# Optimization experiments

Measured on AMD Instinct MI355X. Metric: run time of the kernel, lower is better.

## Reference

```python
import jax, jax.numpy as jnp
import numpy as np

N_HEAD = 16
LN_EPS = 1e-5


def setup_inputs() -> dict:
    key = jax.random.key(0)
    ks = jax.random.split(key, 12)
    B, S, D = 4, 1024, 1024
    s = 1.0 / np.sqrt(D)
    return {
        "Q": jax.random.normal(ks[0], (B, S, D), jnp.float32),
        "K": jax.random.normal(ks[1], (B, S, D), jnp.float32),
        "V": jax.random.normal(ks[2], (B, S, D), jnp.float32),
        # Linear weights stored torch-style [out, in]
        "Wq": jax.random.normal(ks[3], (D, D), jnp.float32) * s,
        "bq": jnp.zeros((D,), jnp.float32),
        "Wk": jax.random.normal(ks[4], (D, D), jnp.float32) * s,
        "bk": jnp.zeros((D,), jnp.float32),
        "Wv": jax.random.normal(ks[5], (D, D), jnp.float32) * s,
        "bv": jnp.zeros((D,), jnp.float32),
        "Wo": jax.random.normal(ks[6], (D, D), jnp.float32) * s,
        "bo": jnp.zeros((D,), jnp.float32),
        "ln_g": jnp.ones((D,), jnp.float32),
        "ln_b": jnp.zeros((D,), jnp.float32),
    }


def _layer_norm(x, g, b):
    mu = jnp.mean(x, axis=-1, keepdims=True)
    var = jnp.mean(jnp.square(x - mu), axis=-1, keepdims=True)
    return (x - mu) * jax.lax.rsqrt(var + LN_EPS) * g + b


def reference(Q, K, V, Wq, bq, Wk, bk, Wv, bv, Wo, bo, ln_g, ln_b):
    B, S, D = Q.shape
    H = N_HEAD
    dk = D // H
    # projections, split heads: [B, H, S, dk]
    q = (Q @ Wq.T + bq).reshape(B, S, H, dk).transpose(0, 2, 1, 3)
    k = (K @ Wk.T + bk).reshape(B, S, H, dk).transpose(0, 2, 1, 3)
    v = (V @ Wv.T + bv).reshape(B, S, H, dk).transpose(0, 2, 1, 3)
    scores = jnp.einsum("bhqd,bhkd->bhqk", q, k) / np.sqrt(dk)
    # NOTE: original module applies softmax twice (F.softmax then nn.Softmax)
    attn = jax.nn.softmax(jax.nn.softmax(scores, axis=-1), axis=-1)
    ctx = jnp.einsum("bhqk,bhkd->bhqd", attn, v)  # [B, H, S, dk]
    ctx = ctx.transpose(0, 2, 1, 3).reshape(B, S, D)
    out = ctx @ Wo.T + bo
    return _layer_norm(out + Q, ln_g, ln_b)
```

## Files before the change

kernel.cpp:

```cpp
#include <hip/hip_runtime.h>
#include <cstdint>
#include <cstddef>


typedef unsigned short ushort_t;
typedef __attribute__((ext_vector_type(8))) short bf16x8;
typedef __attribute__((ext_vector_type(8))) unsigned short us8;
typedef __attribute__((ext_vector_type(4))) unsigned short us4;
typedef __attribute__((ext_vector_type(4))) float f32x4;

#define MFMA16(a, b, c) __builtin_amdgcn_mfma_f32_16x16x32_bf16((a), (b), (c), 0, 0, 0)

__device__ __forceinline__ float b2f(ushort_t u) {
  union { unsigned int i; float f; } x; x.i = ((unsigned int)u) << 16; return x.f;
}
__device__ __forceinline__ ushort_t f2b(float f) {
  union { unsigned int i; float f; } x; x.f = f;
  unsigned int r = (x.i + 0x7FFFu + ((x.i >> 16) & 1u)) >> 16;
  return (ushort_t)r;
}
__device__ __forceinline__ us8 cvt8(float4 a, float4 b) {
  us8 r;
  r[0] = f2b(a.x); r[1] = f2b(a.y); r[2] = f2b(a.z); r[3] = f2b(a.w);
  r[4] = f2b(b.x); r[5] = f2b(b.y); r[6] = f2b(b.z); r[7] = f2b(b.w);
  return r;
}

__device__ __forceinline__ void gll16(const ushort_t* g, ushort_t* l) {
  __builtin_amdgcn_global_load_lds(
      (const __attribute__((address_space(1))) void*)g,
      (__attribute__((address_space(3))) void*)l, 16, 0, 0);
}

__global__ __launch_bounds__(256, 8) void cvt4_kernel(
    const float* __restrict__ w0, const float* __restrict__ w1,
    const float* __restrict__ w2, const float* __restrict__ w3,
    ushort_t* __restrict__ dst) {
  const int which = blockIdx.y;
  const float* src = (which == 0) ? w0 : (which == 1) ? w1 : (which == 2) ? w2 : w3;
  const int i = (blockIdx.x * 256 + threadIdx.x) * 8;
  const float4 a = *(const float4*)(src + i);
  const float4 b = *(const float4*)(src + i + 4);
  *(us8*)(dst + (size_t)which * 1048576 + i) = cvt8(a, b);
}

__global__ __launch_bounds__(256, 3) void qkv_proj_kernel(
    const float* __restrict__ Qin, const float* __restrict__ Kin,
    const float* __restrict__ Vin,
    const ushort_t* __restrict__ wq, const ushort_t* __restrict__ wk,
    const ushort_t* __restrict__ wv,
    const float* __restrict__ bq, const float* __restrict__ bk,
    const float* __restrict__ bv,
    ushort_t* __restrict__ qb, ushort_t* __restrict__ kb,
    ushort_t* __restrict__ vb) {
  __shared__ __align__(16) ushort_t Asl[128 * 32];
  __shared__ __align__(16) ushort_t Bsl[128 * 32];
  const float* A; const ushort_t* W; const float* bias; float scale;
  if (blockIdx.z == 0)      { A = Qin; W = wq; bias = bq; scale = 0.125f; }
  else if (blockIdx.z == 1) { A = Kin; W = wk; bias = bk; scale = 1.0f; }
  else                      { A = Vin; W = wv; bias = bv; scale = 1.0f; }
  const int l = blockIdx.x;
  const int xcd = l & 7, ii = l >> 3;
  const int m0 = (xcd * 4 + (ii >> 3)) * 128;
  const int n0 = (ii & 7) * 128;
  const int tid = threadIdx.x;
  const int wave = tid >> 6, lane = tid & 63;
  const int l15 = lane & 15, quad = lane >> 4;
  const int wr = wave >> 1, wc = wave & 1;

  const int ra = tid >> 2, ca = (tid & 3) * 8;
  const float* Ap0 = A + (size_t)(m0 + ra) * 1024 + ca;
  const float* Ap1 = A + (size_t)(m0 + ra + 64) * 1024 + ca;

  const int rB0 = wave * 32 + (lane >> 2);
  const ushort_t* Bg0 = W + (size_t)(n0 + rB0) * 1024 + (lane & 3) * 8;
  const ushort_t* Bg1 = W + (size_t)(n0 + rB0 + 16) * 1024 + (lane & 3) * 8;
  ushort_t* Bl0 = Bsl + wave * 1024;
  ushort_t* Bl1 = Bsl + wave * 1024 + 512;

  float4 a00 = *(const float4*)(Ap0), a01 = *(const float4*)(Ap0 + 4);
  float4 a10 = *(const float4*)(Ap1), a11 = *(const float4*)(Ap1 + 4);

  f32x4 acc[4][4] = {};
  for (int k0 = 0; k0 < 1024; k0 += 32) {
    __syncthreads();
    *(us8*)(Asl + ra * 32 + ca) = cvt8(a00, a01);
    *(us8*)(Asl + (ra + 64) * 32 + ca) = cvt8(a10, a11);
    gll16(Bg0 + k0, Bl0);
    gll16(Bg1 + k0, Bl1);
    __syncthreads();
    if (k0 + 32 < 1024) {
      a00 = *(const float4*)(Ap0 + k0 + 32); a01 = *(const float4*)(Ap0 + k0 + 36);
      a10 = *(const float4*)(Ap1 + k0 + 32); a11 = *(const float4*)(Ap1 + k0 + 36);
    }
    bf16x8 af[4], bfr[4];
#pragma unroll
    for (int s = 0; s < 4; ++s)
      af[s] = *(const bf16x8*)(Asl + (wr * 64 + s * 16 + l15) * 32 + quad * 8);
#pragma unroll
    for (int s = 0; s < 4; ++s)
      bfr[s] = *(const bf16x8*)(Bsl + (wc * 64 + s * 16 + l15) * 32 + quad * 8);
#pragma unroll
    for (int ms = 0; ms < 4; ++ms)
#pragma unroll
      for (int ns = 0; ns < 4; ++ns)
        acc[ms][ns] = MFMA16(af[ms], bfr[ns], acc[ms][ns]);
  }

  if (blockIdx.z != 2) {
    ushort_t* outp = (blockIdx.z == 0) ? qb : kb;
#pragma unroll
    for (int ns = 0; ns < 4; ++ns) {
      const int col = n0 + wc * 64 + ns * 16 + l15;
      const float bv_ = bias[col];
#pragma unroll
      for (int ms = 0; ms < 4; ++ms) {
        const int rowb = m0 + wr * 64 + ms * 16 + quad * 4;
#pragma unroll
        for (int r = 0; r < 4; ++r) {
          outp[(size_t)(rowb + r) * 1024 + col] =
              f2b((acc[ms][ns][r] + bv_) * scale);
        }
      }
    }
  } else {
#pragma unroll
    for (int ns = 0; ns < 4; ++ns) {
      const int col = n0 + wc * 64 + ns * 16 + l15;
      const float bv_ = bias[col];
      const int h = col >> 6, d = col & 63;
#pragma unroll
      for (int ms = 0; ms < 4; ++ms) {
        const int i0 = m0 + wr * 64 + ms * 16 + quad * 4;
        const int b = i0 >> 10, s0 = i0 & 1023;
        us4 pack;
#pragma unroll
        for (int r = 0; r < 4; ++r) pack[r] = f2b(acc[ms][ns][r] + bv_);
        *(us4*)(vb + ((size_t)(b * 16 + h) * 64 + d) * 1024 + s0) = pack;
      }
    }
  }
}

__global__ __launch_bounds__(256, 4) void attn_kernel(
    const ushort_t* __restrict__ qb, const ushort_t* __restrict__ kb,
    const ushort_t* __restrict__ vb, ushort_t* __restrict__ ctx) {
  __shared__ __align__(16) ushort_t Qs[64 * 72];
  __shared__ __align__(16) ushort_t Ks[64 * 72];
  __shared__ __align__(16) ushort_t Vt[64 * 72];
  __shared__ __align__(16) ushort_t Ps[4][16 * 68];

  const int tid = threadIdx.x, wave = tid >> 6, lane = tid & 63;
  const int l15 = lane & 15, quad = lane >> 4;
  const int l = blockIdx.x;
  const int xcd = l & 7, ii = l >> 3;
  const int bh = xcd * 8 + (ii >> 4);
  const int q0 = (ii & 15) * 64;
  const int b = bh >> 4, h = bh & 15;
  const ushort_t* qg = qb + ((size_t)b << 20) + h * 64;
  const ushort_t* kg = kb + ((size_t)b << 20) + h * 64;
  const ushort_t* vg = vb + ((size_t)bh << 16);

  const int kr0 = tid >> 3, kc0 = (tid & 7) * 8;
  const int kr1 = (tid + 256) >> 3, kc1 = kc0;

  *(us8*)(Qs + kr0 * 72 + kc0) = *(const us8*)(qg + (size_t)(q0 + kr0) * 1024 + kc0);
  *(us8*)(Qs + kr1 * 72 + kc1) = *(const us8*)(qg + (size_t)(q0 + kr1) * 1024 + kc1);

  float z1[4] = {0.f, 0.f, 0.f, 0.f};
  us8 rk0 = *(const us8*)(kg + (size_t)kr0 * 1024 + kc0);
  us8 rk1 = *(const us8*)(kg + (size_t)kr1 * 1024 + kc1);
  for (int kt = 0; kt < 16; ++kt) {
    __syncthreads();
    *(us8*)(Ks + kr0 * 72 + kc0) = rk0;
    *(us8*)(Ks + kr1 * 72 + kc1) = rk1;
    __syncthreads();
    if (kt < 15) {
      rk0 = *(const us8*)(kg + (size_t)((kt + 1) * 64 + kr0) * 1024 + kc0);
      rk1 = *(const us8*)(kg + (size_t)((kt + 1) * 64 + kr1) * 1024 + kc1);
    }
    f32x4 sc[4] = {};
#pragma unroll
    for (int kk = 0; kk < 2; ++kk) {
      const bf16x8 aq = *(const bf16x8*)(Qs + (wave * 16 + l15) * 72 + kk * 32 + quad * 8);
#pragma unroll
      for (int ns = 0; ns < 4; ++ns) {
        const bf16x8 bk_ = *(const bf16x8*)(Ks + (ns * 16 + l15) * 72 + kk * 32 + quad * 8);
        sc[ns] = MFMA16(aq, bk_, sc[ns]);
      }
    }
#pragma unroll
    for (int ns = 0; ns < 4; ++ns)
#pragma unroll
      for (int r = 0; r < 4; ++r) z1[r] += __expf(sc[ns][r]);
  }
  float iz1[4];
#pragma unroll
  for (int r = 0; r < 4; ++r) {
    float s = z1[r];
#pragma unroll
    for (int off = 1; off < 16; off <<= 1) s += __shfl_xor(s, off, 64);
    iz1[r] = 1.0f / s;
  }

  f32x4 oac[4] = {};
  float z2[4] = {0.f, 0.f, 0.f, 0.f};
  rk0 = *(const us8*)(kg + (size_t)kr0 * 1024 + kc0);
  rk1 = *(const us8*)(kg + (size_t)kr1 * 1024 + kc1);
  us8 rv0 = *(const us8*)(vg + (size_t)kr0 * 1024 + kc0);
  us8 rv1 = *(const us8*)(vg + (size_t)kr1 * 1024 + kc1);
  for (int kt = 0; kt < 16; ++kt) {
    __syncthreads();
    *(us8*)(Ks + kr0 * 72 + kc0) = rk0;
    *(us8*)(Ks + kr1 * 72 + kc1) = rk1;
    *(us8*)(Vt + kr0 * 72 + kc0) = rv0;
    *(us8*)(Vt + kr1 * 72 + kc1) = rv1;
    __syncthreads();
    if (kt < 15) {
      rk0 = *(const us8*)(kg + (size_t)((kt + 1) * 64 + kr0) * 1024 + kc0);
      rk1 = *(const us8*)(kg + (size_t)((kt + 1) * 64 + kr1) * 1024 + kc1);
      rv0 = *(const us8*)(vg + (size_t)kr0 * 1024 + (kt + 1) * 64 + kc0);
      rv1 = *(const us8*)(vg + (size_t)kr1 * 1024 + (kt + 1) * 64 + kc1);
    }
    f32x4 sc[4] = {};
#pragma unroll
    for (int kk = 0; kk < 2; ++kk) {
      const bf16x8 aq = *(const bf16x8*)(Qs + (wave * 16 + l15) * 72 + kk * 32 + quad * 8);
#pragma unroll
      for (int ns = 0; ns < 4; ++ns) {
        const bf16x8 bk_ = *(const bf16x8*)(Ks + (ns * 16 + l15) * 72 + kk * 32 + quad * 8);
        sc[ns] = MFMA16(aq, bk_, sc[ns]);
      }
    }
#pragma unroll
    for (int ns = 0; ns < 4; ++ns)
#pragma unroll
      for (int r = 0; r < 4; ++r) {
        const float p1 = __expf(sc[ns][r]) * iz1[r];
        const float e2 = __expf(p1);
        z2[r] += e2;
        Ps[wave][(quad * 4 + r) * 68 + ns * 16 + l15] = f2b(e2);
      }
    __asm__ __volatile__("s_waitcnt lgkmcnt(0)" ::: "memory");
#pragma unroll
    for (int kk = 0; kk < 2; ++kk) {
      const ushort_t* pp = &Ps[wave][l15 * 68 + kk * 32 + quad * 8];
      union { us4 hseg[2]; bf16x8 v; } u;
      u.hseg[0] = *(const us4*)pp;
      u.hseg[1] = *(const us4*)(pp + 4);
      const bf16x8 ap = u.v;
#pragma unroll
      for (int ns2 = 0; ns2 < 4; ++ns2) {
        const bf16x8 bv_ = *(const bf16x8*)(Vt + (ns2 * 16 + l15) * 72 + kk * 32 + quad * 8);
        oac[ns2] = MFMA16(ap, bv_, oac[ns2]);
      }
    }
  }

#pragma unroll
  for (int r = 0; r < 4; ++r) {
    float s = z2[r];
#pragma unroll
    for (int off = 1; off < 16; off <<= 1) s += __shfl_xor(s, off, 64);
    z2[r] = s;
  }
#pragma unroll
  for (int ns2 = 0; ns2 < 4; ++ns2) {
    const int d = ns2 * 16 + l15;
#pragma unroll
    for (int r = 0; r < 4; ++r) {
      const int s = q0 + wave * 16 + quad * 4 + r;
      ctx[((size_t)(b * 1024 + s)) * 1024 + h * 64 + d] = f2b(oac[ns2][r] / z2[r]);
    }
  }
}

__global__ __launch_bounds__(256, 3) void out_proj_kernel(
    const ushort_t* __restrict__ ctxp, const ushort_t* __restrict__ wo,
    const float* __restrict__ bo, ushort_t* __restrict__ pre) {
  __shared__ __align__(16) ushort_t Asl[128 * 32];
  __shared__ __align__(16) ushort_t Bsl[128 * 32];
  const int tid = threadIdx.x;
  const int wave = tid >> 6, lane = tid & 63;
  const int l15 = lane & 15, quad = lane >> 4;
  const int wr = wave >> 1, wc = wave & 1;
  const int l = blockIdx.x;
  const int xcd = l & 7, ii = l >> 3;
  const int m0 = (xcd * 4 + (ii >> 3)) * 128;
  const int n0 = (ii & 7) * 128;

  const int rr = wave * 32 + (lane >> 2);
  const int cc = (lane & 3) * 8;
  const ushort_t* Ag0 = ctxp + (size_t)(m0 + rr) * 1024 + cc;
  const ushort_t* Ag1 = ctxp + (size_t)(m0 + rr + 16) * 1024 + cc;
  const ushort_t* Bg0 = wo + (size_t)(n0 + rr) * 1024 + cc;
  const ushort_t* Bg1 = wo + (size_t)(n0 + rr + 16) * 1024 + cc;
  ushort_t* Al0 = Asl + wave * 1024;
  ushort_t* Al1 = Asl + wave * 1024 + 512;
  ushort_t* Bl0 = Bsl + wave * 1024;
  ushort_t* Bl1 = Bsl + wave * 1024 + 512;

  f32x4 acc[4][4] = {};
  for (int k0 = 0; k0 < 1024; k0 += 32) {
    __syncthreads();
    gll16(Ag0 + k0, Al0);
    gll16(Ag1 + k0, Al1);
    gll16(Bg0 + k0, Bl0);
    gll16(Bg1 + k0, Bl1);
    __syncthreads();
    bf16x8 af[4], bfr[4];
#pragma unroll
    for (int s = 0; s < 4; ++s)
      af[s] = *(const bf16x8*)(Asl + (wr * 64 + s * 16 + l15) * 32 + quad * 8);
#pragma unroll
    for (int s = 0; s < 4; ++s)
      bfr[s] = *(const bf16x8*)(Bsl + (wc * 64 + s * 16 + l15) * 32 + quad * 8);
#pragma unroll
    for (int ms = 0; ms < 4; ++ms)
#pragma unroll
      for (int ns = 0; ns < 4; ++ns)
        acc[ms][ns] = MFMA16(af[ms], bfr[ns], acc[ms][ns]);
  }

#pragma unroll
  for (int ns = 0; ns < 4; ++ns) {
    const int col = n0 + wc * 64 + ns * 16 + l15;
    const float bv_ = bo[col];
#pragma unroll
    for (int ms = 0; ms < 4; ++ms) {
      const int rowb = m0 + wr * 64 + ms * 16 + quad * 4;
#pragma unroll
      for (int r = 0; r < 4; ++r) {
        pre[(size_t)(rowb + r) * 1024 + col] = f2b(acc[ms][ns][r] + bv_);
      }
    }
  }
}

__global__ __launch_bounds__(256, 4) void ln_kernel(
    const ushort_t* __restrict__ pre, const float* __restrict__ Q,
    const float* __restrict__ g, const float* __restrict__ bta,
    float* __restrict__ out) {
  const int row = blockIdx.x;
  const int tid = threadIdx.x;
  const size_t base = (size_t)row * 1024 + tid * 4;
  const ushort4 p4 = *(const ushort4*)(pre + base);
  const float4 q4 = *(const float4*)(Q + base);
  float v[4] = {b2f(p4.x) + q4.x, b2f(p4.y) + q4.y,
                b2f(p4.z) + q4.z, b2f(p4.w) + q4.w};
  float s1 = v[0] + v[1] + v[2] + v[3];
  float s2 = v[0]*v[0] + v[1]*v[1] + v[2]*v[2] + v[3]*v[3];
#pragma unroll
  for (int off = 1; off < 64; off <<= 1) {
    s1 += __shfl_xor(s1, off, 64);
    s2 += __shfl_xor(s2, off, 64);
  }
  __shared__ float r1[4], r2[4];
  const int wave = tid >> 6, lane = tid & 63;
  if (lane == 0) { r1[wave] = s1; r2[wave] = s2; }
  __syncthreads();
  const float t1 = r1[0] + r1[1] + r1[2] + r1[3];
  const float t2 = r2[0] + r2[1] + r2[2] + r2[3];
  const float mu = t1 * (1.0f / 1024.0f);
  const float var = t2 * (1.0f / 1024.0f) - mu * mu;
  const float inv = rsqrtf(var + 1e-5f);
  const int c0 = tid * 4;
#pragma unroll
  for (int j = 0; j < 4; ++j) {
    const int c = c0 + j;
    out[(size_t)row * 1024 + c] = (v[j] - mu) * inv * g[c] + bta[c];
  }
}

extern "C" void kernel_launch(void* const* d_in, const int* in_sizes, int n_in,
                              void* d_out, int out_size, void* d_ws, size_t ws_size,
                              hipStream_t stream) {
  const float* Q  = (const float*)d_in[0];
  const float* K  = (const float*)d_in[1];
  const float* V  = (const float*)d_in[2];
  const float* Wq = (const float*)d_in[3];
  const float* bq = (const float*)d_in[4];
  const float* Wk = (const float*)d_in[5];
  const float* bk = (const float*)d_in[6];
  const float* Wv = (const float*)d_in[7];
  const float* bv = (const float*)d_in[8];
  const float* Wo = (const float*)d_in[9];
  const float* bo = (const float*)d_in[10];
  const float* lg = (const float*)d_in[11];
  const float* lb = (const float*)d_in[12];

  char* ws = (char*)d_ws;
  ushort_t* qb  = (ushort_t*)(ws);
  ushort_t* kb  = (ushort_t*)(ws + ((size_t)8  << 20));
  ushort_t* vb  = (ushort_t*)(ws + ((size_t)16 << 20));
  ushort_t* pre = (ushort_t*)(ws);

  ushort_t* dptr  = (ushort_t*)d_out;
  ushort_t* wo_bf = dptr;
  ushort_t* wq_bf = dptr + 1048576;
  ushort_t* wk_bf = dptr + 2097152;
  ushort_t* wv_bf = dptr + 3145728;
  ushort_t* ctx   = dptr + 4194304;
  float*    out   = (float*)d_out;

  cvt4_kernel<<<dim3(512, 4), 256, 0, stream>>>(Wo, Wq, Wk, Wv, dptr);
  qkv_proj_kernel<<<dim3(256, 1, 3), 256, 0, stream>>>(Q, K, V, wq_bf, wk_bf, wv_bf,
                                                       bq, bk, bv, qb, kb, vb);
  attn_kernel<<<dim3(1024), 256, 0, stream>>>(qb, kb, vb, ctx);
  out_proj_kernel<<<dim3(256), 256, 0, stream>>>(ctx, wo_bf, bo, pre);
  ln_kernel<<<dim3(4096), 256, 0, stream>>>(pre, Q, lg, lb, out);
}
```

Before: 247.0 us.

## Double-buffer projection GEMMs, use exp2 softmax, hoist Q fragments, shrink out-proj tiles

The QKV and output projection GEMMs now use two LDS buffers with 64-wide k steps, so the next tile loads while the current one is computed and one barrier per stage is dropped. The output projection tile shrinks to 64x128 with twice as many blocks and a higher occupancy hint, which spreads work over more CUs. The attention kernel folds log2(e) into the Q scale and first-softmax normaliser so it can call hardware exp2 directly, and it keeps the Q MFMA fragments in registers instead of re-reading them from LDS every iteration. Double buffering doubles LDS per block and adds register pressure, which may lower occupancy.

```diff
diff --git a/kernel.cpp b/kernel.cpp
--- a/kernel.cpp
+++ b/kernel.cpp
@@ -10,6 +10,8 @@
 typedef __attribute__((ext_vector_type(4))) float f32x4;
 
 #define MFMA16(a, b, c) __builtin_amdgcn_mfma_f32_16x16x32_bf16((a), (b), (c), 0, 0, 0)
+#define EXP2F(x) __builtin_amdgcn_exp2f(x)
+#define LOG2E 1.4426950408889634f
 
 __device__ __forceinline__ float b2f(ushort_t u) {
   union { unsigned int i; float f; } x; x.i = ((unsigned int)u) << 16; return x.f;
@@ -53,10 +55,12 @@
     const float* __restrict__ bv,
     ushort_t* __restrict__ qb, ushort_t* __restrict__ kb,
     ushort_t* __restrict__ vb) {
-  __shared__ __align__(16) ushort_t Asl[128 * 32];
-  __shared__ __align__(16) ushort_t Bsl[128 * 32];
+  __shared__ __align__(16) ushort_t Asl0[128 * 32];
+  __shared__ __align__(16) ushort_t Asl1[128 * 32];
+  __shared__ __align__(16) ushort_t Bsl0[128 * 32];
+  __shared__ __align__(16) ushort_t Bsl1[128 * 32];
   const float* A; const ushort_t* W; const float* bias; float scale;
-  if (blockIdx.z == 0)      { A = Qin; W = wq; bias = bq; scale = 0.125f; }
+  if (blockIdx.z == 0)      { A = Qin; W = wq; bias = bq; scale = 0.125f * LOG2E; }
   else if (blockIdx.z == 1) { A = Kin; W = wk; bias = bk; scale = 1.0f; }
   else                      { A = Vin; W = wv; bias = bv; scale = 1.0f; }
   const int l = blockIdx.x;
@@ -72,40 +76,59 @@
   const float* Ap0 = A + (size_t)(m0 + ra) * 1024 + ca;
   const float* Ap1 = A + (size_t)(m0 + ra + 64) * 1024 + ca;
 
-  const int rB0 = wave * 32 + (lane >> 2);
-  const ushort_t* Bg0 = W + (size_t)(n0 + rB0) * 1024 + (lane & 3) * 8;
-  const ushort_t* Bg1 = W + (size_t)(n0 + rB0 + 16) * 1024 + (lane & 3) * 8;
-  ushort_t* Bl0 = Bsl + wave * 1024;
-  ushort_t* Bl1 = Bsl + wave * 1024 + 512;
-
-  float4 a00 = *(const float4*)(Ap0), a01 = *(const float4*)(Ap0 + 4);
-  float4 a10 = *(const float4*)(Ap1), a11 = *(const float4*)(Ap1 + 4);
+  const ushort_t* Bg0 = W + (size_t)(n0 + wave * 32 + (lane >> 2)) * 1024 + (lane & 3) * 8;
+  const ushort_t* Bg1 = W + (size_t)(n0 + wave * 32 + 16 + (lane >> 2)) * 1024 + (lane & 3) * 8;
+
+  float4 xa0 = *(const float4*)(Ap0), xa1 = *(const float4*)(Ap0 + 4);
+  float4 xa2 = *(const float4*)(Ap1), xa3 = *(const float4*)(Ap1 + 4);
+  gll16(Bg0, Bsl0 + wave * 1024);
+  gll16(Bg1, Bsl0 + wave * 1024 + 512);
+  *(us8*)(Asl0 + ra * 32 + ca) = cvt8(xa0, xa1);
+  *(us8*)(Asl0 + (ra + 64) * 32 + ca) = cvt8(xa2, xa3);
+  float4 ya0 = *(const float4*)(Ap0 + 32), ya1 = *(const float4*)(Ap0 + 36);
+  float4 ya2 = *(const float4*)(Ap1 + 32), ya3 = *(const float4*)(Ap1 + 36);
+  __syncthreads();
 
   f32x4 acc[4][4] = {};
-  for (int k0 = 0; k0 < 1024; k0 += 32) {
-    __syncthreads();
-    *(us8*)(Asl + ra * 32 + ca) = cvt8(a00, a01);
-    *(us8*)(Asl + (ra + 64) * 32 + ca) = cvt8(a10, a11);
-    gll16(Bg0 + k0, Bl0);
-    gll16(Bg1 + k0, Bl1);
-    __syncthreads();
-    if (k0 + 32 < 1024) {
-      a00 = *(const float4*)(Ap0 + k0 + 32); a01 = *(const float4*)(Ap0 + k0 + 36);
-      a10 = *(const float4*)(Ap1 + k0 + 32); a11 = *(const float4*)(Ap1 + k0 + 36);
-    }
-    bf16x8 af[4], bfr[4];
-#pragma unroll
-    for (int s = 0; s < 4; ++s)
-      af[s] = *(const bf16x8*)(Asl + (wr * 64 + s * 16 + l15) * 32 + quad * 8);
-#pragma unroll
-    for (int s = 0; s < 4; ++s)
-      bfr[s] = *(const bf16x8*)(Bsl + (wc * 64 + s * 16 + l15) * 32 + quad * 8);
-#pragma unroll
-    for (int ms = 0; ms < 4; ++ms)
-#pragma unroll
-      for (int ns = 0; ns < 4; ++ns)
-        acc[ms][ns] = MFMA16(af[ms], bfr[ns], acc[ms][ns]);
-  }
+#define QKV_COMPUTE(ASL, BSL)                                                   \
+  {                                                                             \
+    bf16x8 af[4], bfr[4];                                                       \
+    _Pragma("unroll") for (int s = 0; s < 4; ++s)                               \
+        af[s] = *(const bf16x8*)((ASL) + (wr * 64 + s * 16 + l15) * 32 + quad * 8); \
+    _Pragma("unroll") for (int s = 0; s < 4; ++s)                               \
+        bfr[s] = *(const bf16x8*)((BSL) + (wc * 64 + s * 16 + l15) * 32 + quad * 8); \
+    _Pragma("unroll") for (int ms = 0; ms < 4; ++ms)                            \
+        _Pragma("unroll") for (int ns = 0; ns < 4; ++ns)                        \
+            acc[ms][ns] = MFMA16(af[ms], bfr[ns], acc[ms][ns]);                 \
+  }
+
+  for (int k0 = 0; k0 < 1024; k0 += 64) {
+    {
+      gll16(Bg0 + k0 + 32, Bsl1 + wave * 1024);
+      gll16(Bg1 + k0 + 32, Bsl1 + wave * 1024 + 512);
+      *(us8*)(Asl1 + ra * 32 + ca) = cvt8(ya0, ya1);
+      *(us8*)(Asl1 + (ra + 64) * 32 + ca) = cvt8(ya2, ya3);
+    }
+    if (k0 + 64 < 1024) {
+      xa0 = *(const float4*)(Ap0 + k0 + 64); xa1 = *(const float4*)(Ap0 + k0 + 68);
+      xa2 = *(const float4*)(Ap1 + k0 + 64); xa3 = *(const float4*)(Ap1 + k0 + 68);
+    }
+    QKV_COMPUTE(Asl0, Bsl0)
+    __syncthreads();
+    if (k0 + 64 < 1024) {
+      gll16(Bg0 + k0 + 64, Bsl0 + wave * 1024);
+      gll16(Bg1 + k0 + 64, Bsl0 + wave * 1024 + 512);
+      *(us8*)(Asl0 + ra * 32 + ca) = cvt8(xa0, xa1);
+      *(us8*)(Asl0 + (ra + 64) * 32 + ca) = cvt8(xa2, xa3);
+      if (k0 + 96 < 1024) {
+        ya0 = *(const float4*)(Ap0 + k0 + 96); ya1 = *(const float4*)(Ap0 + k0 + 100);
+        ya2 = *(const float4*)(Ap1 + k0 + 96); ya3 = *(const float4*)(Ap1 + k0 + 100);
+      }
+    }
+    QKV_COMPUTE(Asl1, Bsl1)
+    __syncthreads();
+  }
+#undef QKV_COMPUTE
 
   if (blockIdx.z != 2) {
     ushort_t* outp = (blockIdx.z == 0) ? qb : kb;
@@ -166,6 +189,10 @@
 
   *(us8*)(Qs + kr0 * 72 + kc0) = *(const us8*)(qg + (size_t)(q0 + kr0) * 1024 + kc0);
   *(us8*)(Qs + kr1 * 72 + kc1) = *(const us8*)(qg + (size_t)(q0 + kr1) * 1024 + kc1);
+  __syncthreads();
+  bf16x8 aqh[2];
+  aqh[0] = *(const bf16x8*)(Qs + (wave * 16 + l15) * 72 + quad * 8);
+  aqh[1] = *(const bf16x8*)(Qs + (wave * 16 + l15) * 72 + 32 + quad * 8);
 
   float z1[4] = {0.f, 0.f, 0.f, 0.f};
   us8 rk0 = *(const us8*)(kg + (size_t)kr0 * 1024 + kc0);
@@ -182,17 +209,16 @@
     f32x4 sc[4] = {};
 #pragma unroll
     for (int kk = 0; kk < 2; ++kk) {
-      const bf16x8 aq = *(const bf16x8*)(Qs + (wave * 16 + l15) * 72 + kk * 32 + quad * 8);
 #pragma unroll
       for (int ns = 0; ns < 4; ++ns) {
         const bf16x8 bk_ = *(const bf16x8*)(Ks + (ns * 16 + l15) * 72 + kk * 32 + quad * 8);
-        sc[ns] = MFMA16(aq, bk_, sc[ns]);
+        sc[ns] = MFMA16(aqh[kk], bk_, sc[ns]);
       }
     }
 #pragma unroll
     for (int ns = 0; ns < 4; ++ns)
 #pragma unroll
-      for (int r = 0; r < 4; ++r) z1[r] += __expf(sc[ns][r]);
+      for (int r = 0; r < 4; ++r) z1[r] += EXP2F(sc[ns][r]);
   }
   float iz1[4];
 #pragma unroll
@@ -200,7 +226,7 @@
     float s = z1[r];
 #pragma unroll
     for (int off = 1; off < 16; off <<= 1) s += __shfl_xor(s, off, 64);
-    iz1[r] = 1.0f / s;
+    iz1[r] = LOG2E / s;
   }
 
   f32x4 oac[4] = {};
@@ -225,19 +251,18 @@
     f32x4 sc[4] = {};
 #pragma unroll
     for (int kk = 0; kk < 2; ++kk) {
-      const bf16x8 aq = *(const bf16x8*)(Qs + (wave * 16 + l15) * 72 + kk * 32 + quad * 8);
 #pragma unroll
       for (int ns = 0; ns < 4; ++ns) {
         const bf16x8 bk_ = *(const bf16x8*)(Ks + (ns * 16 + l15) * 72 + kk * 32 + quad * 8);
-        sc[ns] = MFMA16(aq, bk_, sc[ns]);
+        sc[ns] = MFMA16(aqh[kk], bk_, sc[ns]);
       }
     }
 #pragma unroll
     for (int ns = 0; ns < 4; ++ns)
 #pragma unroll
       for (int r = 0; r < 4; ++r) {
-        const float p1 = __expf(sc[ns][r]) * iz1[r];
-        const float e2 = __expf(p1);
+        const float p1 = EXP2F(sc[ns][r]) * iz1[r];
+        const float e2 = EXP2F(p1);
         z2[r] += e2;
         Ps[wave][(quad * 4 + r) * 68 + ns * 16 + l15] = f2b(e2);
       }
@@ -275,60 +300,69 @@
   }
 }
 
-__global__ __launch_bounds__(256, 3) void out_proj_kernel(
+__global__ __launch_bounds__(256, 4) void out_proj_kernel(
     const ushort_t* __restrict__ ctxp, const ushort_t* __restrict__ wo,
     const float* __restrict__ bo, ushort_t* __restrict__ pre) {
-  __shared__ __align__(16) ushort_t Asl[128 * 32];
-  __shared__ __align__(16) ushort_t Bsl[128 * 32];
+  __shared__ __align__(16) ushort_t Asl0[64 * 32];
+  __shared__ __align__(16) ushort_t Asl1[64 * 32];
+  __shared__ __align__(16) ushort_t Bsl0[128 * 32];
+  __shared__ __align__(16) ushort_t Bsl1[128 * 32];
   const int tid = threadIdx.x;
   const int wave = tid >> 6, lane = tid & 63;
   const int l15 = lane & 15, quad = lane >> 4;
   const int wr = wave >> 1, wc = wave & 1;
   const int l = blockIdx.x;
   const int xcd = l & 7, ii = l >> 3;
-  const int m0 = (xcd * 4 + (ii >> 3)) * 128;
+  const int m0 = (xcd * 8 + (ii >> 3)) * 64;
   const int n0 = (ii & 7) * 128;
 
-  const int rr = wave * 32 + (lane >> 2);
-  const int cc = (lane & 3) * 8;
-  const ushort_t* Ag0 = ctxp + (size_t)(m0 + rr) * 1024 + cc;
-  const ushort_t* Ag1 = ctxp + (size_t)(m0 + rr + 16) * 1024 + cc;
-  const ushort_t* Bg0 = wo + (size_t)(n0 + rr) * 1024 + cc;
-  const ushort_t* Bg1 = wo + (size_t)(n0 + rr + 16) * 1024 + cc;
-  ushort_t* Al0 = Asl + wave * 1024;
-  ushort_t* Al1 = Asl + wave * 1024 + 512;
-  ushort_t* Bl0 = Bsl + wave * 1024;
-  ushort_t* Bl1 = Bsl + wave * 1024 + 512;
-
-  f32x4 acc[4][4] = {};
-  for (int k0 = 0; k0 < 1024; k0 += 32) {
-    __syncthreads();
-    gll16(Ag0 + k0, Al0);
-    gll16(Ag1 + k0, Al1);
-    gll16(Bg0 + k0, Bl0);
-    gll16(Bg1 + k0, Bl1);
-    __syncthreads();
-    bf16x8 af[4], bfr[4];
-#pragma unroll
-    for (int s = 0; s < 4; ++s)
-      af[s] = *(const bf16x8*)(Asl + (wr * 64 + s * 16 + l15) * 32 + quad * 8);
-#pragma unroll
-    for (int s = 0; s < 4; ++s)
-      bfr[s] = *(const bf16x8*)(Bsl + (wc * 64 + s * 16 + l15) * 32 + quad * 8);
-#pragma unroll
-    for (int ms = 0; ms < 4; ++ms)
-#pragma unroll
-      for (int ns = 0; ns < 4; ++ns)
-        acc[ms][ns] = MFMA16(af[ms], bfr[ns], acc[ms][ns]);
-  }
+  const ushort_t* Ag = ctxp + (size_t)(m0 + wave * 16 + (lane >> 2)) * 1024 + (lane & 3) * 8;
+  const ushort_t* Bg0 = wo + (size_t)(n0 + wave * 32 + (lane >> 2)) * 1024 + (lane & 3) * 8;
+  const ushort_t* Bg1 = wo + (size_t)(n0 + wave * 32 + 16 + (lane >> 2)) * 1024 + (lane & 3) * 8;
+
+  gll16(Ag, Asl0 + wave * 512);
+  gll16(Bg0, Bsl0 + wave * 1024);
+  gll16(Bg1, Bsl0 + wave * 1024 + 512);
+  __syncthreads();
+
+  f32x4 acc[2][4] = {};
+#define OUTP_COMPUTE(ASL, BSL)                                                  \
+  {                                                                             \
+    bf16x8 af[2], bfr[4];                                                       \
+    _Pragma("unroll") for (int s = 0; s < 2; ++s)                               \
+        af[s] = *(const bf16x8*)((ASL) + (wr * 32 + s * 16 + l15) * 32 + quad * 8); \
+    _Pragma("unroll") for (int s = 0; s < 4; ++s)                               \
+        bfr[s] = *(const bf16x8*)((BSL) + (wc * 64 + s * 16 + l15) * 32 + quad * 8); \
+    _Pragma("unroll") for (int ms = 0; ms < 2; ++ms)                            \
+        _Pragma("unroll") for (int ns = 0; ns < 4; ++ns)                        \
+            acc[ms][ns] = MFMA16(af[ms], bfr[ns], acc[ms][ns]);                 \
+  }
+
+  for (int k0 = 0; k0 < 1024; k0 += 64) {
+    {
+      gll16(Ag + k0 + 32, Asl1 + wave * 512);
+      gll16(Bg0 + k0 + 32, Bsl1 + wave * 1024);
+      gll16(Bg1 + k0 + 32, Bsl1 + wave * 1024 + 512);
+    }
+    OUTP_COMPUTE(Asl0, Bsl0)
+    __syncthreads();
+    if (k0 + 64 < 1024) {
+      gll16(Ag + k0 + 64, Asl0 + wave * 512);
+      gll16(Bg0 + k0 + 64, Bsl0 + wave * 1024);
+      gll16(Bg1 + k0 + 64, Bsl0 + wave * 1024 + 512);
+    }
+    OUTP_COMPUTE(Asl1, Bsl1)
+    __syncthreads();
+  }
+#undef OUTP_COMPUTE
 
 #pragma unroll
   for (int ns = 0; ns < 4; ++ns) {
     const int col = n0 + wc * 64 + ns * 16 + l15;
     const float bv_ = bo[col];
 #pragma unroll
-    for (int ms = 0; ms < 4; ++ms) {
-      const int rowb = m0 + wr * 64 + ms * 16 + quad * 4;
+    for (int ms = 0; ms < 2; ++ms) {
+      const int rowb = m0 + wr * 32 + ms * 16 + quad * 4;
 #pragma unroll
       for (int r = 0; r < 4; ++r) {
         pre[(size_t)(rowb + r) * 1024 + col] = f2b(acc[ms][ns][r] + bv_);
@@ -407,6 +441,6 @@
   qkv_proj_kernel<<<dim3(256, 1, 3), 256, 0, stream>>>(Q, K, V, wq_bf, wk_bf, wv_bf,
                                                        bq, bk, bv, qb, kb, vb);
   attn_kernel<<<dim3(1024), 256, 0, stream>>>(qb, kb, vb, ctx);
-  out_proj_kernel<<<dim3(256), 256, 0, stream>>>(ctx, wo_bf, bo, pre);
+  out_proj_kernel<<<dim3(512), 256, 0, stream>>>(ctx, wo_bf, bo, pre);
   ln_kernel<<<dim3(4096), 256, 0, stream>>>(pre, Q, lg, lb, out);
 }
```

New measurement: 240.1 us. -2.8%, faster.
